# Kernel optimization log

Hardware: AMD Instinct MI355X
Metric: run time of the kernel (lower is better)

Reference implementation:

```python
import jax, jax.numpy as jnp
import numpy as np

T, B, D = 2048, 2, 768
H = 8
HD = D // H
FFN = 3072
EPS = 1e-5


def layer_norm(x, g, b):
    mu = jnp.mean(x, axis=-1, keepdims=True)
    var = jnp.mean(jnp.square(x - mu), axis=-1, keepdims=True)
    return (x - mu) * jax.lax.rsqrt(var + EPS) * g + b


def setup_inputs() -> dict:
    key = jax.random.key(0)
    ks = jax.random.split(key, 12)
    s_d = 1.0 / np.sqrt(D)
    s_f = 1.0 / np.sqrt(FFN)
    return {
        "x": jax.random.normal(ks[0], (T, B, D), dtype=jnp.float32),
        "wq": jax.random.uniform(ks[1], (D, D), jnp.float32, -s_d, s_d),
        "bq": jnp.zeros((D,), jnp.float32),
        "wk": jax.random.uniform(ks[2], (D, D), jnp.float32, -s_d, s_d),
        "bk": jnp.zeros((D,), jnp.float32),
        "wv": jax.random.uniform(ks[3], (D, D), jnp.float32, -s_d, s_d),
        "bv": jnp.zeros((D,), jnp.float32),
        "wo": jax.random.uniform(ks[4], (D, D), jnp.float32, -s_d, s_d),
        "bo": jnp.zeros((D,), jnp.float32),
        "ln1_g": jnp.ones((D,), jnp.float32),
        "ln1_b": jnp.zeros((D,), jnp.float32),
        "w1": jax.random.uniform(ks[5], (FFN, D), jnp.float32, -s_d, s_d),
        "b1": jnp.zeros((FFN,), jnp.float32),
        "w2": jax.random.uniform(ks[6], (D, FFN), jnp.float32, -s_f, s_f),
        "b2": jnp.zeros((D,), jnp.float32),
        "ln2_g": jnp.ones((D,), jnp.float32),
        "ln2_b": jnp.zeros((D,), jnp.float32),
    }


def reference(x, wq, bq, wk, bk, wv, bv, wo, bo, ln1_g, ln1_b, w1, b1, w2, b2, ln2_g, ln2_b):
    # x: [T, B, D] (fairseq layout). Post-LN (layer_norm_first=False), relu, eval mode.
    residual = x
    q = (x @ wq.T + bq).reshape(T, B, H, HD)
    k = (x @ wk.T + bk).reshape(T, B, H, HD)
    v = (x @ wv.T + bv).reshape(T, B, H, HD)
    scale = 1.0 / np.sqrt(HD)
    scores = jnp.einsum('tbhd,sbhd->bhts', q, k) * scale  # [B,H,T,T]
    probs = jax.nn.softmax(scores, axis=-1)
    attn = jnp.einsum('bhts,sbhd->tbhd', probs, v).reshape(T, B, D)
    attn = attn @ wo.T + bo
    x = layer_norm(residual + attn, ln1_g, ln1_b)
    residual = x
    h = jax.nn.relu(x @ w1.T + b1)
    x = residual + (h @ w2.T + b2)
    x = layer_norm(x, ln2_g, ln2_b)
    return x
```

## Files before the change

### kernel.cpp

```cpp
#include <hip/hip_runtime.h>
#include <hip/hip_bf16.h>
#include <math.h>

constexpr int T_LEN = 2048;
constexpr int B_SZ  = 2;
constexpr int D_DIM = 768;
constexpr int H_NUM = 8;
constexpr int HD    = 96;
constexpr int FFN   = 3072;
constexpr float EPS = 1e-5f;
constexpr int TB    = T_LEN * B_SZ;
constexpr int QKV_LD = 3 * D_DIM;
constexpr int NSPLIT = 4;
constexpr int CHUNK  = T_LEN / NSPLIT;
constexpr float SC_LOG2E = 0.14724444458547f;

typedef __attribute__((ext_vector_type(8)))  short short8;
typedef __attribute__((ext_vector_type(4)))  short short4v;
typedef __attribute__((ext_vector_type(4)))  float f32x4;
typedef __attribute__((ext_vector_type(16))) float f32x16;

__device__ __forceinline__ short f2bf(float f) {
    union { float f; unsigned u; } v; v.f = f;
    return (short)((v.u + 0x7FFFu + ((v.u >> 16) & 1u)) >> 16);
}
__device__ __forceinline__ float bf2f(short s) {
    union { unsigned u; float f; } v;
    v.u = ((unsigned)(unsigned short)s) << 16;
    return v.f;
}
__device__ __forceinline__ unsigned pkbf(float a, float b) {
    union { __hip_bfloat162 h; unsigned u; } v;
    v.h = __float22bfloat162_rn(make_float2(a, b));
    return v.u;
}

__device__ __forceinline__ void async_ld16(const short* g, short* l) {
    __builtin_amdgcn_global_load_lds(
        (const __attribute__((address_space(1))) unsigned int*)g,
        (__attribute__((address_space(3))) unsigned int*)l, 16, 0, 0);
}

struct CvtArgs {
    const float* src[7];
    short*       dst[7];
    float        scl[7];
    int          end4[7];
};

__global__ __launch_bounds__(256)
void cvt_all(CvtArgs a, int total4) {
    const int i = blockIdx.x * 256 + threadIdx.x;
    if (i >= total4) return;
    int s = 0;
    while (i >= a.end4[s]) ++s;
    const int base = s ? a.end4[s - 1] : 0;
    const int j = i - base;
    const float sc = a.scl[s];
    const float4 v = ((const float4*)a.src[s])[j];
    short4v o;
    o[0] = f2bf(v.x * sc); o[1] = f2bf(v.y * sc);
    o[2] = f2bf(v.z * sc); o[3] = f2bf(v.w * sc);
    *(short4v*)(a.dst[s] + (size_t)j * 4) = o;
}

__global__ __launch_bounds__(256)
void concat_bias(const float* __restrict__ bq, const float* __restrict__ bk,
                 const float* __restrict__ bv, float* __restrict__ dst) {
    const int i = blockIdx.x * 256 + threadIdx.x;
    if (i >= QKV_LD) return;
    dst[i] = (i < 768) ? bq[i] * SC_LOG2E : (i < 1536 ? bk[i - 768] : bv[i - 1536]);
}

template <int BN, typename OutT, bool RELU>
__global__ __launch_bounds__(256)
void gemm_mfma(const short* __restrict__ A, const short* __restrict__ W,
               const float* __restrict__ bias, OutT* __restrict__ C,
               int M, int N, int K) {
    constexpr int NI = BN / 32;
    __shared__ __align__(16) short As[128 * 32];
    __shared__ __align__(16) short Bs[BN * 32];

    const int tid  = threadIdx.x;
    const int w    = tid >> 6;
    const int lane = tid & 63;
    const int l16  = lane & 15;
    const int q4   = lane >> 4;
    const int row0 = blockIdx.y * 128;
    const int col0 = blockIdx.x * BN;
    const int wm   = (w >> 1) * 64;
    const int wn   = (w & 1) * (BN / 2);

    const short* gA0 = A + (size_t)(row0 + (tid >> 2)) * K + (tid & 3) * 8;
    const short* gA1 = gA0 + (size_t)64 * K;
    const short* gB0 = W + (size_t)(col0 + (tid >> 2)) * K + (tid & 3) * 8;
    const short* gB1 = gB0 + (size_t)64 * K;
    short* ldsA0 = As + w * 512;
    short* ldsA1 = As + 2048 + w * 512;
    short* ldsB0 = Bs + w * 512;
    short* ldsB1 = Bs + 2048 + w * 512;

    f32x4 acc[4][NI];
#pragma unroll
    for (int mi = 0; mi < 4; ++mi)
#pragma unroll
        for (int ni = 0; ni < NI; ++ni)
#pragma unroll
            for (int r = 0; r < 4; ++r) acc[mi][ni][r] = 0.f;

    for (int k0 = 0; k0 < K; k0 += 32) {
        async_ld16(gA0, ldsA0);
        async_ld16(gA1, ldsA1);
        async_ld16(gB0, ldsB0);
        if constexpr (BN == 128) async_ld16(gB1, ldsB1);
        gA0 += 32; gA1 += 32; gB0 += 32;
        if constexpr (BN == 128) gB1 += 32;
        __syncthreads();

        short8 af[4], bfr[NI];
#pragma unroll
        for (int mi = 0; mi < 4; ++mi)
            af[mi] = *(const short8*)&As[(wm + mi * 16 + l16) * 32 + q4 * 8];
#pragma unroll
        for (int ni = 0; ni < NI; ++ni)
            bfr[ni] = *(const short8*)&Bs[(wn + ni * 16 + l16) * 32 + q4 * 8];
#pragma unroll
        for (int mi = 0; mi < 4; ++mi)
#pragma unroll
            for (int ni = 0; ni < NI; ++ni)
                acc[mi][ni] = __builtin_amdgcn_mfma_f32_16x16x32_bf16(
                    af[mi], bfr[ni], acc[mi][ni], 0, 0, 0);
        __syncthreads();
    }

    float bcol[NI];
#pragma unroll
    for (int ni = 0; ni < NI; ++ni) bcol[ni] = bias[col0 + wn + ni * 16 + l16];
#pragma unroll
    for (int mi = 0; mi < 4; ++mi) {
#pragma unroll
        for (int r = 0; r < 4; ++r) {
            const int row = row0 + wm + mi * 16 + q4 * 4 + r;
#pragma unroll
            for (int ni = 0; ni < NI; ++ni) {
                float v = acc[mi][ni][r] + bcol[ni];
                if (RELU) v = fmaxf(v, 0.f);
                const int col = col0 + wn + ni * 16 + l16;
                if constexpr (sizeof(OutT) == 2)
                    C[(size_t)row * N + col] = (OutT)f2bf(v);
                else
                    C[(size_t)row * N + col] = v;
            }
        }
    }
}

__global__ __launch_bounds__(128)
void attn_mfma(const short* __restrict__ qkv, short* __restrict__ Opart,
               float* __restrict__ lpart) {
    __shared__ short Ks[32][112];
    __shared__ short Vt[128][44];
    __shared__ short Pw[2][32][36];

    const int tid  = threadIdx.x;
    const int w    = tid >> 6;
    const int lane = tid & 63;
    const int l31  = lane & 31;
    const int h5   = lane >> 5;
    const int t0   = blockIdx.x * 64;
    const int bh   = blockIdx.y;
    const int split = blockIdx.z;
    const int b    = bh >> 3;
    const int h    = bh & 7;

    for (int i = tid; i < 32 * 44; i += 128) {
        const int rr = i / 44, cc = i % 44;
        Vt[96 + rr][cc] = (rr == 0 && cc < 32) ? (short)0x3F80 : (short)0;
    }

    short8 qf[6];
    {
        const int qrow = t0 + w * 32 + l31;
        const short* qb = qkv + ((size_t)qrow * B_SZ + b) * QKV_LD + h * HD;
#pragma unroll
        for (int ks = 0; ks < 6; ++ks)
            qf[ks] = *(const short8*)&qb[ks * 16 + h5 * 8];
    }

    const int k_row = lane >> 1;
    const int k_off = (lane & 1) * 48;
    const short* gK = qkv + ((size_t)(split * CHUNK + k_row) * B_SZ + b) * QKV_LD
                      + D_DIM + h * HD + k_off;
    const int dg = (lane & 7) * 12;
    const int kg = (lane >> 3) * 4;
    const short* gV = qkv + ((size_t)(split * CHUNK + kg) * B_SZ + b) * QKV_LD
                      + 2 * D_DIM + h * HD + dg;
    const size_t step  = (size_t)32 * B_SZ * QKV_LD;
    const size_t vrow  = (size_t)B_SZ * QKV_LD;

    f32x16 oacc[4];
#pragma unroll
    for (int nt = 0; nt < 4; ++nt)
#pragma unroll
        for (int r = 0; r < 16; ++r) oacc[nt][r] = 0.f;

    short8  kpf[6];
    short4v vpf[4][3];
    if (w == 0) {
#pragma unroll
        for (int j = 0; j < 6; ++j) kpf[j] = *(const short8*)(gK + j * 8);
    } else {
#pragma unroll
        for (int r = 0; r < 4; ++r)
#pragma unroll
            for (int c = 0; c < 3; ++c)
                vpf[r][c] = *(const short4v*)(gV + r * vrow + c * 4);
    }

    for (int it = 0; it < CHUNK / 32; ++it) {
        __syncthreads();
        if (w == 0) {
#pragma unroll
            for (int j = 0; j < 6; ++j)
                *(short8*)&Ks[k_row][k_off + j * 8] = kpf[j];
        } else {
#pragma unroll
            for (int d = 0; d < 12; ++d) {
                short4v t;
                t[0] = vpf[0][d >> 2][d & 3];
                t[1] = vpf[1][d >> 2][d & 3];
                t[2] = vpf[2][d >> 2][d & 3];
                t[3] = vpf[3][d >> 2][d & 3];
                *(short4v*)&Vt[dg + d][kg] = t;
            }
        }
        __syncthreads();

        if (it + 1 < CHUNK / 32) {
            const size_t off = (size_t)(it + 1) * step;
            if (w == 0) {
#pragma unroll
                for (int j = 0; j < 6; ++j)
                    kpf[j] = *(const short8*)(gK + off + j * 8);
            } else {
#pragma unroll
                for (int r = 0; r < 4; ++r)
#pragma unroll
                    for (int c = 0; c < 3; ++c)
                        vpf[r][c] = *(const short4v*)(gV + off + r * vrow + c * 4);
            }
        }

        f32x16 sa;
#pragma unroll
        for (int r = 0; r < 16; ++r) sa[r] = 0.f;
#pragma unroll
        for (int ks = 0; ks < 6; ++ks) {
            const short8 kf = *(const short8*)&Ks[l31][ks * 16 + h5 * 8];
            sa = __builtin_amdgcn_mfma_f32_32x32x16_bf16(qf[ks], kf, sa, 0, 0, 0);
        }

        float pvx[16];
#pragma unroll
        for (int r = 0; r < 16; ++r) pvx[r] = __builtin_amdgcn_exp2f(sa[r]);
#pragma unroll
        for (int rp = 0; rp < 8; ++rp) {
            const unsigned u = pkbf(pvx[2 * rp], pvx[2 * rp + 1]);
            const int row = ((2 * rp) & 3) + 8 * ((2 * rp) >> 2) + 4 * h5;
            Pw[w][row][l31]     = (short)(u & 0xFFFFu);
            Pw[w][row + 1][l31] = (short)(u >> 16);
        }

#pragma unroll
        for (int ks2 = 0; ks2 < 2; ++ks2) {
            const short* pp = &Pw[w][l31][ks2 * 16 + h5 * 8];
            const short4v plo = *(const short4v*)pp;
            const short4v phi = *(const short4v*)(pp + 4);
            const short8 pfr = __builtin_shufflevector(plo, phi, 0, 1, 2, 3, 4, 5, 6, 7);
#pragma unroll
            for (int nt = 0; nt < 4; ++nt) {
                const short* vp = &Vt[nt * 32 + l31][ks2 * 16 + h5 * 8];
                const short4v vlo = *(const short4v*)vp;
                const short4v vhi = *(const short4v*)(vp + 4);
                const short8 vf = __builtin_shufflevector(vlo, vhi, 0, 1, 2, 3, 4, 5, 6, 7);
                oacc[nt] = __builtin_amdgcn_mfma_f32_32x32x16_bf16(pfr, vf, oacc[nt], 0, 0, 0);
            }
        }
    }

#pragma unroll
    for (int r = 0; r < 16; ++r) {
        const int row  = (r & 3) + 8 * (r >> 2) + 4 * h5;
        const int t    = t0 + w * 32 + row;
        const int grow = t * B_SZ + b;
        short* op = Opart + ((size_t)split * TB + grow) * D_DIM + h * HD;
#pragma unroll
        for (int nt = 0; nt < 3; ++nt)
            op[nt * 32 + l31] = f2bf(oacc[nt][r]);
        if (l31 == 0)
            lpart[((size_t)split * TB + grow) * H_NUM + h] = oacc[3][r];
    }
}

__global__ __launch_bounds__(256)
void attn_combine(const short* __restrict__ Opart, const float* __restrict__ lpart,
                  short* __restrict__ ctx) {
    const int row = blockIdx.x;
    const int tid = threadIdx.x;
    if (tid >= 192) return;
    const int d = tid * 4;
    const int h = d / 96;
    float o0 = 0.f, o1 = 0.f, o2 = 0.f, o3 = 0.f, l = 0.f;
#pragma unroll
    for (int c = 0; c < NSPLIT; ++c) {
        const short4v v = *(const short4v*)&Opart[((size_t)c * TB + row) * D_DIM + d];
        o0 += bf2f(v[0]); o1 += bf2f(v[1]); o2 += bf2f(v[2]); o3 += bf2f(v[3]);
        l += lpart[((size_t)c * TB + row) * H_NUM + h];
    }
    const float iv = 1.f / l;
    short4v r;
    r[0] = f2bf(o0 * iv); r[1] = f2bf(o1 * iv);
    r[2] = f2bf(o2 * iv); r[3] = f2bf(o3 * iv);
    *(short4v*)&ctx[(size_t)row * D_DIM + d] = r;
}

template <typename XT, typename OT>
__global__ __launch_bounds__(256)
void ln_residual(const XT* __restrict__ xres, const short* __restrict__ y,
                 const float* __restrict__ g, const float* __restrict__ bb,
                 OT* __restrict__ out) {
    const int row = blockIdx.x;
    const int tid = threadIdx.x;
    const XT*    xr = xres + (size_t)row * D_DIM;
    const short* yr = y + (size_t)row * D_DIM;

    float vals[3];
    float s = 0.f, s2 = 0.f;
#pragma unroll
    for (int i = 0; i < 3; ++i) {
        const int d = tid + i * 256;
        float xv;
        if constexpr (sizeof(XT) == 2) xv = bf2f((short)xr[d]);
        else                           xv = (float)xr[d];
        const float t = xv + bf2f(yr[d]);
        vals[i] = t;
        s += t;
        s2 = fmaf(t, t, s2);
    }
#pragma unroll
    for (int off = 32; off > 0; off >>= 1) {
        s  += __shfl_down(s, off);
        s2 += __shfl_down(s2, off);
    }
    __shared__ float red_s[4], red_s2[4];
    const int wid = tid >> 6, lane = tid & 63;
    if (lane == 0) { red_s[wid] = s; red_s2[wid] = s2; }
    __syncthreads();
    __shared__ float sh_mean, sh_rstd;
    if (tid == 0) {
        const float ts  = red_s[0] + red_s[1] + red_s[2] + red_s[3];
        const float ts2 = red_s2[0] + red_s2[1] + red_s2[2] + red_s2[3];
        const float mean = ts * (1.f / D_DIM);
        const float var  = ts2 * (1.f / D_DIM) - mean * mean;
        sh_mean = mean;
        sh_rstd = rsqrtf(var + EPS);
    }
    __syncthreads();
    const float mean = sh_mean, rstd = sh_rstd;
#pragma unroll
    for (int i = 0; i < 3; ++i) {
        const int d = tid + i * 256;
        const float o = (vals[i] - mean) * rstd * g[d] + bb[d];
        if constexpr (sizeof(OT) == 2)
            out[(size_t)row * D_DIM + d] = (OT)f2bf(o);
        else
            out[(size_t)row * D_DIM + d] = o;
    }
}

extern "C" void kernel_launch(void* const* d_in, const int* in_sizes, int n_in,
                              void* d_out, int out_size, void* d_ws, size_t ws_size,
                              hipStream_t stream) {
    const float* x     = (const float*)d_in[0];
    const float* wq    = (const float*)d_in[1];
    const float* bq    = (const float*)d_in[2];
    const float* wk    = (const float*)d_in[3];
    const float* bk    = (const float*)d_in[4];
    const float* wv    = (const float*)d_in[5];
    const float* bv    = (const float*)d_in[6];
    const float* wo    = (const float*)d_in[7];
    const float* bo    = (const float*)d_in[8];
    const float* ln1g  = (const float*)d_in[9];
    const float* ln1b  = (const float*)d_in[10];
    const float* w1    = (const float*)d_in[11];
    const float* b1    = (const float*)d_in[12];
    const float* w2    = (const float*)d_in[13];
    const float* b2    = (const float*)d_in[14];
    const float* ln2g  = (const float*)d_in[15];
    const float* ln2b  = (const float*)d_in[16];
    float* out = (float*)d_out;

    char* ws = (char*)d_ws;
    short* qkvb  = (short*)(ws + 0);
    short* ctxb  = (short*)(ws + 18874368);
    short* hb    = (short*)(ws + 0);
    short* xb    = (short*)(ws + 25165824);
    short* Opart = (short*)(ws + 25165824);
    float* lpart = (float*)(ws + 50331648);
    short* tmpb  = (short*)(ws + 25165824);
    short* x1b   = (short*)(ws + 31457280);
    short* wqkv  = (short*)(ws + 50855936);
    short* wob   = (short*)(ws + 54394880);
    short* w1b   = (short*)(ws + 55574528);
    short* w2b   = (short*)(ws + 60293120);
    float* bqkv  = (float*)(ws + 65011712);

    CvtArgs ca;
    ca.src[0] = x;  ca.dst[0] = xb;   ca.scl[0] = 1.f;
    ca.src[1] = wq; ca.dst[1] = wqkv; ca.scl[1] = SC_LOG2E;
    ca.src[2] = wk; ca.dst[2] = wqkv + 768 * 768;     ca.scl[2] = 1.f;
    ca.src[3] = wv; ca.dst[3] = wqkv + 2 * 768 * 768; ca.scl[3] = 1.f;
    ca.src[4] = wo; ca.dst[4] = wob;  ca.scl[4] = 1.f;
    ca.src[5] = w1; ca.dst[5] = w1b;  ca.scl[5] = 1.f;
    ca.src[6] = w2; ca.dst[6] = w2b;  ca.scl[6] = 1.f;
    const int n4[7] = {TB * D_DIM / 4, 768 * 768 / 4, 768 * 768 / 4, 768 * 768 / 4,
                       768 * 768 / 4, FFN * 768 / 4, 768 * FFN / 4};
    int acc4 = 0;
    for (int i = 0; i < 7; ++i) { acc4 += n4[i]; ca.end4[i] = acc4; }
    cvt_all<<<(acc4 + 255) / 256, 256, 0, stream>>>(ca, acc4);
    concat_bias<<<(QKV_LD + 255) / 256, 256, 0, stream>>>(bq, bk, bv, bqkv);

    gemm_mfma<128, short, false><<<dim3(QKV_LD / 128, TB / 128), 256, 0, stream>>>(
        xb, wqkv, bqkv, qkvb, TB, QKV_LD, D_DIM);

    attn_mfma<<<dim3(T_LEN / 64, B_SZ * H_NUM, NSPLIT), dim3(128), 0, stream>>>(
        qkvb, Opart, lpart);
    attn_combine<<<dim3(TB), 256, 0, stream>>>(Opart, lpart, ctxb);

    gemm_mfma<64, short, false><<<dim3(D_DIM / 64, TB / 128), 256, 0, stream>>>(
        ctxb, wob, bo, tmpb, TB, D_DIM, D_DIM);
    ln_residual<float, short><<<dim3(TB), 256, 0, stream>>>(x, tmpb, ln1g, ln1b, x1b);

    gemm_mfma<128, short, true><<<dim3(FFN / 128, TB / 128), 256, 0, stream>>>(
        x1b, w1b, b1, hb, TB, FFN, D_DIM);
    gemm_mfma<64, short, false><<<dim3(D_DIM / 64, TB / 128), 256, 0, stream>>>(
        hb, w2b, b2, tmpb, TB, D_DIM, FFN);
    ln_residual<short, float><<<dim3(TB), 256, 0, stream>>>(x1b, tmpb, ln2g, ln2b, out);
}
```

Measured before the change: 332.4 us.

## Double-buffer GEMM LDS tiles and split attention K tile to cut bank conflicts

```diff
diff --git a/kernel.cpp b/kernel.cpp
--- a/kernel.cpp
+++ b/kernel.cpp
@@ -78,8 +78,8 @@
                const float* __restrict__ bias, OutT* __restrict__ C,
                int M, int N, int K) {
     constexpr int NI = BN / 32;
-    __shared__ __align__(16) short As[128 * 32];
-    __shared__ __align__(16) short Bs[BN * 32];
+    __shared__ __align__(16) short As[2][128 * 32];
+    __shared__ __align__(16) short Bs[2][BN * 32];
 
     const int tid  = threadIdx.x;
     const int w    = tid >> 6;
@@ -95,10 +95,6 @@
     const short* gA1 = gA0 + (size_t)64 * K;
     const short* gB0 = W + (size_t)(col0 + (tid >> 2)) * K + (tid & 3) * 8;
     const short* gB1 = gB0 + (size_t)64 * K;
-    short* ldsA0 = As + w * 512;
-    short* ldsA1 = As + 2048 + w * 512;
-    short* ldsB0 = Bs + w * 512;
-    short* ldsB1 = Bs + 2048 + w * 512;
 
     f32x4 acc[4][NI];
 #pragma unroll
@@ -108,28 +104,38 @@
 #pragma unroll
             for (int r = 0; r < 4; ++r) acc[mi][ni][r] = 0.f;
 
-    for (int k0 = 0; k0 < K; k0 += 32) {
-        async_ld16(gA0, ldsA0);
-        async_ld16(gA1, ldsA1);
-        async_ld16(gB0, ldsB0);
-        if constexpr (BN == 128) async_ld16(gB1, ldsB1);
+    auto stage = [&](int buf) {
+        async_ld16(gA0, &As[buf][w * 512]);
+        async_ld16(gA1, &As[buf][2048 + w * 512]);
+        async_ld16(gB0, &Bs[buf][w * 512]);
+        if constexpr (BN == 128) async_ld16(gB1, &Bs[buf][2048 + w * 512]);
         gA0 += 32; gA1 += 32; gB0 += 32;
         if constexpr (BN == 128) gB1 += 32;
-        __syncthreads();
-
+    };
+    auto compute = [&](int buf) {
         short8 af[4], bfr[NI];
 #pragma unroll
         for (int mi = 0; mi < 4; ++mi)
-            af[mi] = *(const short8*)&As[(wm + mi * 16 + l16) * 32 + q4 * 8];
+            af[mi] = *(const short8*)&As[buf][(wm + mi * 16 + l16) * 32 + q4 * 8];
 #pragma unroll
         for (int ni = 0; ni < NI; ++ni)
-            bfr[ni] = *(const short8*)&Bs[(wn + ni * 16 + l16) * 32 + q4 * 8];
+            bfr[ni] = *(const short8*)&Bs[buf][(wn + ni * 16 + l16) * 32 + q4 * 8];
 #pragma unroll
         for (int mi = 0; mi < 4; ++mi)
 #pragma unroll
             for (int ni = 0; ni < NI; ++ni)
                 acc[mi][ni] = __builtin_amdgcn_mfma_f32_16x16x32_bf16(
                     af[mi], bfr[ni], acc[mi][ni], 0, 0, 0);
+    };
+
+    stage(0);
+    __syncthreads();
+    for (int k0 = 0; k0 < K; k0 += 64) {
+        stage(1);
+        compute(0);
+        __syncthreads();
+        if (k0 + 64 < K) stage(0);
+        compute(1);
         __syncthreads();
     }
 
@@ -158,7 +164,7 @@
 __global__ __launch_bounds__(128)
 void attn_mfma(const short* __restrict__ qkv, short* __restrict__ Opart,
                float* __restrict__ lpart) {
-    __shared__ short Ks[32][112];
+    __shared__ short Ks[2][32][56];
     __shared__ short Vt[128][44];
     __shared__ short Pw[2][32][36];
 
@@ -188,9 +194,9 @@
     }
 
     const int k_row = lane >> 1;
-    const int k_off = (lane & 1) * 48;
+    const int k_half = lane & 1;
     const short* gK = qkv + ((size_t)(split * CHUNK + k_row) * B_SZ + b) * QKV_LD
-                      + D_DIM + h * HD + k_off;
+                      + D_DIM + h * HD + k_half * 48;
     const int dg = (lane & 7) * 12;
     const int kg = (lane >> 3) * 4;
     const short* gV = qkv + ((size_t)(split * CHUNK + kg) * B_SZ + b) * QKV_LD
@@ -222,7 +228,7 @@
         if (w == 0) {
 #pragma unroll
             for (int j = 0; j < 6; ++j)
-                *(short8*)&Ks[k_row][k_off + j * 8] = kpf[j];
+                *(short8*)&Ks[k_half][k_row][j * 8] = kpf[j];
         } else {
 #pragma unroll
             for (int d = 0; d < 12; ++d) {
@@ -256,7 +262,9 @@
         for (int r = 0; r < 16; ++r) sa[r] = 0.f;
 #pragma unroll
         for (int ks = 0; ks < 6; ++ks) {
-            const short8 kf = *(const short8*)&Ks[l31][ks * 16 + h5 * 8];
+            const int half = ks / 3;
+            const int base = ks * 16 - half * 48;
+            const short8 kf = *(const short8*)&Ks[half][l31][base + h5 * 8];
             sa = __builtin_amdgcn_mfma_f32_32x32x16_bf16(qf[ks], kf, sa, 0, 0, 0);
         }
 
```

Measured after the change: 352.9 us. 1.06x slower.

## Double attention block to four waves sharing each K/V tile

Applied to the files above, without the earlier changes.

```diff
diff --git a/kernel.cpp b/kernel.cpp
--- a/kernel.cpp
+++ b/kernel.cpp
@@ -17,6 +17,7 @@
 
 typedef __attribute__((ext_vector_type(8)))  short short8;
 typedef __attribute__((ext_vector_type(4)))  short short4v;
+typedef __attribute__((ext_vector_type(2)))  short short2v;
 typedef __attribute__((ext_vector_type(4)))  float f32x4;
 typedef __attribute__((ext_vector_type(16))) float f32x16;
 
@@ -155,25 +156,25 @@
     }
 }
 
-__global__ __launch_bounds__(128)
+__global__ __launch_bounds__(256)
 void attn_mfma(const short* __restrict__ qkv, short* __restrict__ Opart,
                float* __restrict__ lpart) {
-    __shared__ short Ks[32][112];
+    __shared__ short Ks[2][32][56];
     __shared__ short Vt[128][44];
-    __shared__ short Pw[2][32][36];
+    __shared__ short Pw[4][32][36];
 
     const int tid  = threadIdx.x;
     const int w    = tid >> 6;
     const int lane = tid & 63;
     const int l31  = lane & 31;
     const int h5   = lane >> 5;
-    const int t0   = blockIdx.x * 64;
+    const int t0   = blockIdx.x * 128;
     const int bh   = blockIdx.y;
     const int split = blockIdx.z;
     const int b    = bh >> 3;
     const int h    = bh & 7;
 
-    for (int i = tid; i < 32 * 44; i += 128) {
+    for (int i = tid; i < 32 * 44; i += 256) {
         const int rr = i / 44, cc = i % 44;
         Vt[96 + rr][cc] = (rr == 0 && cc < 32) ? (short)0x3F80 : (short)0;
     }
@@ -187,12 +188,13 @@
             qf[ks] = *(const short8*)&qb[ks * 16 + h5 * 8];
     }
 
-    const int k_row = lane >> 1;
-    const int k_off = (lane & 1) * 48;
+    const int k_row = tid >> 2;
+    const int k_q   = tid & 3;
     const short* gK = qkv + ((size_t)(split * CHUNK + k_row) * B_SZ + b) * QKV_LD
-                      + D_DIM + h * HD + k_off;
-    const int dg = (lane & 7) * 12;
-    const int kg = (lane >> 3) * 4;
+                      + D_DIM + h * HD + k_q * 24;
+    const int ll = tid - 128;
+    const int dg = (ll & 7) * 12;
+    const int kg = (ll >> 3) * 2;
     const short* gV = qkv + ((size_t)(split * CHUNK + kg) * B_SZ + b) * QKV_LD
                       + 2 * D_DIM + h * HD + dg;
     const size_t step  = (size_t)32 * B_SZ * QKV_LD;
@@ -204,14 +206,14 @@
 #pragma unroll
         for (int r = 0; r < 16; ++r) oacc[nt][r] = 0.f;
 
-    short8  kpf[6];
-    short4v vpf[4][3];
-    if (w == 0) {
-#pragma unroll
-        for (int j = 0; j < 6; ++j) kpf[j] = *(const short8*)(gK + j * 8);
+    short8  kpf[3];
+    short4v vpf[2][3];
+    if (w < 2) {
+#pragma unroll
+        for (int j = 0; j < 3; ++j) kpf[j] = *(const short8*)(gK + j * 8);
     } else {
 #pragma unroll
-        for (int r = 0; r < 4; ++r)
+        for (int r = 0; r < 2; ++r)
 #pragma unroll
             for (int c = 0; c < 3; ++c)
                 vpf[r][c] = *(const short4v*)(gV + r * vrow + c * 4);
@@ -219,32 +221,30 @@
 
     for (int it = 0; it < CHUNK / 32; ++it) {
         __syncthreads();
-        if (w == 0) {
-#pragma unroll
-            for (int j = 0; j < 6; ++j)
-                *(short8*)&Ks[k_row][k_off + j * 8] = kpf[j];
+        if (w < 2) {
+#pragma unroll
+            for (int j = 0; j < 3; ++j)
+                *(short8*)&Ks[k_q >> 1][k_row][(k_q & 1) * 24 + j * 8] = kpf[j];
         } else {
 #pragma unroll
             for (int d = 0; d < 12; ++d) {
-                short4v t;
+                short2v t;
                 t[0] = vpf[0][d >> 2][d & 3];
                 t[1] = vpf[1][d >> 2][d & 3];
-                t[2] = vpf[2][d >> 2][d & 3];
-                t[3] = vpf[3][d >> 2][d & 3];
-                *(short4v*)&Vt[dg + d][kg] = t;
+                *(short2v*)&Vt[dg + d][kg] = t;
             }
         }
         __syncthreads();
 
         if (it + 1 < CHUNK / 32) {
             const size_t off = (size_t)(it + 1) * step;
-            if (w == 0) {
-#pragma unroll
-                for (int j = 0; j < 6; ++j)
+            if (w < 2) {
+#pragma unroll
+                for (int j = 0; j < 3; ++j)
                     kpf[j] = *(const short8*)(gK + off + j * 8);
             } else {
 #pragma unroll
-                for (int r = 0; r < 4; ++r)
+                for (int r = 0; r < 2; ++r)
 #pragma unroll
                     for (int c = 0; c < 3; ++c)
                         vpf[r][c] = *(const short4v*)(gV + off + r * vrow + c * 4);
@@ -256,7 +256,9 @@
         for (int r = 0; r < 16; ++r) sa[r] = 0.f;
 #pragma unroll
         for (int ks = 0; ks < 6; ++ks) {
-            const short8 kf = *(const short8*)&Ks[l31][ks * 16 + h5 * 8];
+            const int half = ks / 3;
+            const int base = ks * 16 - half * 48;
+            const short8 kf = *(const short8*)&Ks[half][l31][base + h5 * 8];
             sa = __builtin_amdgcn_mfma_f32_32x32x16_bf16(qf[ks], kf, sa, 0, 0, 0);
         }
 
@@ -433,7 +435,7 @@
     gemm_mfma<128, short, false><<<dim3(QKV_LD / 128, TB / 128), 256, 0, stream>>>(
         xb, wqkv, bqkv, qkvb, TB, QKV_LD, D_DIM);
 
-    attn_mfma<<<dim3(T_LEN / 64, B_SZ * H_NUM, NSPLIT), dim3(128), 0, stream>>>(
+    attn_mfma<<<dim3(T_LEN / 128, B_SZ * H_NUM, NSPLIT), dim3(256), 0, stream>>>(
         qkvb, Opart, lpart);
     attn_combine<<<dim3(TB), 256, 0, stream>>>(Opart, lpart, ctxb);
 
```

Result: faster. 320.9 us (-3.5%).
